# Performance work log

Hardware: AMD Instinct MI355X
Metric: run time of the kernel (lower is better)

The kernel has to match this reference:

```python
import jax, jax.numpy as jnp
import numpy as np

B, T, V, H = 4, 512, 8000, 7


def setup_inputs() -> dict:
    key = jax.random.key(0)
    k1, k2, k3 = jax.random.split(key, 3)
    return {
        "input_ids": jax.random.randint(k1, (B, T), 0, V),
        "frequencies": jax.random.normal(k2, (V,), dtype=jnp.float32) * 3.0,
        "amplitudes": 1.0 + jax.random.normal(k3, (V,), dtype=jnp.float32) * 0.1,
        "decay": jnp.asarray(1.5, dtype=jnp.float32),
        "chunk_size": 16,
    }


def reference(input_ids, frequencies, amplitudes, decay, chunk_size):
    h = jnp.arange(1, H + 1, dtype=frequencies.dtype)  # (H,)
    # harmonic expansion: freqs = f*[1..H], amps = A/[1..H]^decay
    all_f = frequencies[:, None] * h                    # (V, H)
    all_A = amplitudes[:, None] / h ** decay            # (V, H)
    seq_f = frequencies[input_ids][..., None] * h       # (B, T, H)
    seq_A = amplitudes[input_ids][..., None] / h ** decay

    nc = T // chunk_size
    sfc = seq_f.reshape(B, nc, chunk_size, H).transpose(1, 0, 2, 3)  # (nc,B,c,H)
    sAc = seq_A.reshape(B, nc, chunk_size, H).transpose(1, 0, 2, 3)

    def per_chunk(args):
        sf, sA = args  # (B,c,H)
        df = sf[:, :, :, None, None] - all_f[None, None, None, :, :]   # (B,c,H,V,H)
        amp = sA[:, :, :, None, None] * all_A[None, None, None, :, :]
        return 2.0 * (amp * jnp.sinc(2.0 * df)).sum(axis=(2, 4))       # (B,c,V)

    Cc = jax.lax.map(per_chunk, (sfc, sAc))            # (nc, B, c, V)
    C = Cc.transpose(1, 0, 2, 3).reshape(B, T, V)      # (B, T, V)

    cum = jnp.cumsum(C, axis=1)
    # logits[t] uses history 0..t-1 -> shift right by one, position 0 gets zeros
    logits = jnp.concatenate([jnp.zeros_like(cum[:, :1]), cum[:, :-1]], axis=1)
    return logits
```

## Files before the change

### kernel.cpp

```cpp
#include <hip/hip_runtime.h>
#include <math.h>


typedef float v2f __attribute__((ext_vector_type(2)));
typedef float v4f __attribute__((ext_vector_type(4)));

constexpr int cB = 4, cT = 512, cV = 8000, cH = 7;
constexpr int GT = 16;
constexpr int NSEG = cT / GT;

__device__ __forceinline__ v2f pk_add(v2f a, v2f b) {
    v2f d; asm("v_pk_add_f32 %0, %1, %2" : "=v"(d) : "v"(a), "v"(b)); return d;
}
__device__ __forceinline__ v2f pk_mul(v2f a, v2f b) {
    v2f d; asm("v_pk_mul_f32 %0, %1, %2" : "=v"(d) : "v"(a), "v"(b)); return d;
}
__device__ __forceinline__ v2f pk_fma(v2f a, v2f b, v2f c) {
    v2f d; asm("v_pk_fma_f32 %0, %1, %2, %3" : "=v"(d) : "v"(a), "v"(b), "v"(c));
    return d;
}
__device__ __forceinline__ float rfl(float x) {
    return __builtin_bit_cast(float,
        __builtin_amdgcn_readfirstlane(__builtin_bit_cast(int, x)));
}

__global__ __launch_bounds__(256) void wavelm_g(
    const int* __restrict__ ids, const float* __restrict__ freq,
    const float* __restrict__ amp, const float* __restrict__ decay_p,
    float* __restrict__ out, float* __restrict__ segsum, const int segmode)
{
    const int bs  = blockIdx.y;
    const int bt0 = bs * GT;
    if ((blockIdx.x * 256 + (int)(threadIdx.x & 192u)) * 2 >= cV) return;
    const int vh  = blockIdx.x * 256 + threadIdx.x;
    const bool valid = (vh * 2 < cV);
    const int vc = valid ? vh : 0;

    const float decay = decay_p[0];
    const float q2 = __builtin_amdgcn_exp2f(-decay);
    const float q3 = __builtin_amdgcn_exp2f(-decay * 1.5849625007f);
    const float q5 = __builtin_amdgcn_exp2f(-decay * 2.3219280949f);
    const float q7 = __builtin_amdgcn_exp2f(-decay * 2.8073549221f);
    const float rp[7] = {1.f, q2, q3, q2*q2, q5, q2*q3, q7};

    const v2f fv = *(const v2f*)(freq + (size_t)vc * 2);
    const v2f Av = *(const v2f*)(amp  + (size_t)vc * 2);
    v2f nb[cH], sBw[cH], cBw[cH];
    {
        const float xrx = fv.x - rintf(fv.x);
        const float xry = fv.y - rintf(fv.y);
        const float s1x = __builtin_amdgcn_sinf(xrx);
        const float c1x = __builtin_amdgcn_cosf(xrx);
        const float s1y = __builtin_amdgcn_sinf(xry);
        const float c1y = __builtin_amdgcn_cosf(xry);
        float sx = s1x, cx = c1x, sy = s1y, cy = c1y;
#pragma unroll
        for (int k = 0; k < cH; ++k) {
            if (k) {
                const float spx = sx, cpx = cx, spy = sy, cpy = cy;
                sx = fmaf(spx, c1x,  cpx * s1x);
                cx = fmaf(cpx, c1x, -(spx * s1x));
                sy = fmaf(spy, c1y,  cpy * s1y);
                cy = fmaf(cpy, c1y, -(spy * s1y));
            }
            const float wx = Av.x * rp[k];
            const float wy = Av.y * rp[k];
            const float wsx = wx * 0.15915494309189535f;
            const float wsy = wy * 0.15915494309189535f;
            sBw[k].x = sx * wsx;  sBw[k].y = sy * wsy;
            cBw[k].x = cx * wsx;  cBw[k].y = cy * wsy;
            nb[k].x = -(fv.x * (float)(k + 1));
            nb[k].y = -(fv.y * (float)(k + 1));
        }
    }

    v2f acc;  acc.x = 0.f;  acc.y = 0.f;

    int idc = ids[bt0];
    for (int g = 0; g < GT; ++g) {
        const int idn = (g + 1 < GT) ? ids[bt0 + g + 1] : idc;

        const float fu = freq[idc];
        const float Au = amp[idc];
        const float xru = fu - rintf(fu);
        const float s1u = rfl(__builtin_amdgcn_sinf(xru));
        const float c1u = rfl(__builtin_amdgcn_cosf(xru));

        float accx = 0.f, accy = 0.f;
        float su = s1u, cu = c1u;
#pragma unroll
        for (int i = 0; i < cH; ++i) {
            if (i) { const float sp = su, cp = cu;
                     su = fmaf(sp, c1u,  cp * s1u);
                     cu = fmaf(cp, c1u, -(sp * s1u)); }
            const float au = fu * (float)(i + 1);
            v2f ai;  ai.x = au;  ai.y = au;
            v2f d[cH], p[cH];
#pragma unroll
            for (int j = 0; j < cH; ++j) d[j] = pk_add(ai, nb[j]);
            p[0] = d[0];
#pragma unroll
            for (int j = 1; j < cH; ++j) p[j] = pk_mul(p[j-1], d[j]);
            const float ptot = p[6].x * p[6].y;
            const float rt = __builtin_amdgcn_rcpf(ptot);
            v2f r;  r.x = rt * p[6].y;  r.y = rt * p[6].x;
            v2f accS = (v2f)0.f, accC = (v2f)0.f;
#pragma unroll
            for (int j = cH - 1; j >= 1; --j) {
                const v2f inv = pk_mul(r, p[j-1]);
                accS = pk_fma(cBw[j], inv, accS);
                accC = pk_fma(sBw[j], inv, accC);
                r = pk_mul(r, d[j]);
            }
            accS = pk_fma(cBw[0], r, accS);
            accC = pk_fma(sBw[0], r, accC);
            const float tx = fmaf(su, accS.x, -(cu * accC.x));
            const float ty = fmaf(su, accS.y, -(cu * accC.y));
            accx = fmaf(rp[i], tx, accx);
            accy = fmaf(rp[i], ty, accy);
        }

        if (!(fabsf(accx) < 1e30f) || !(fabsf(accy) < 1e30f)) {
            accx = 0.f;  accy = 0.f;
            float s2 = s1u, c2 = c1u;
#pragma unroll
            for (int i = 0; i < cH; ++i) {
                if (i) { const float sp = s2, cp = c2;
                         s2 = fmaf(sp, c1u,  cp * s1u);
                         c2 = fmaf(cp, c1u, -(sp * s1u)); }
                const float au = fu * (float)(i + 1);
                float ax = 0.f, ay = 0.f;
#pragma unroll
                for (int j = 0; j < cH; ++j) {
                    const float wxx = Av.x * rp[j];
                    const float wyy = Av.y * rp[j];
                    const float dx = au + nb[j].x;
                    const float dy = au + nb[j].y;
                    const float snx = fmaf(s2, cBw[j].x, -(c2 * sBw[j].x));
                    const float sny = fmaf(s2, cBw[j].y, -(c2 * sBw[j].y));
                    float qx = snx * __builtin_amdgcn_rcpf(dx);
                    float qy = sny * __builtin_amdgcn_rcpf(dy);
                    qx = (dx == 0.f) ? wxx : qx;
                    qy = (dy == 0.f) ? wyy : qy;
                    ax += qx;  ay += qy;
                }
                accx = fmaf(rp[i], ax, accx);
                accy = fmaf(rp[i], ay, accy);
            }
        }

        if (valid) {
            const float A2 = 2.f * Au;
            v2f res;  res.x = A2 * accx;  res.y = A2 * accy;
            const size_t o = (size_t)(bt0 + g) * cV + (size_t)vh * 2;
            v2f wv;  wv.x = segmode ? acc.x : res.x;
                     wv.y = segmode ? acc.y : res.y;
            *(v2f*)(out + o) = wv;
            acc = pk_add(acc, res);
        }

        idc = idn;
    }

    if (valid && segmode)
        *(v2f*)(segsum + (size_t)bs * cV + (size_t)vh * 2) = acc;
}

__global__ __launch_bounds__(256) void wavelm_addbase(
    float* __restrict__ out, const float* __restrict__ segsum)
{
    const int btq = blockIdx.y;
    const int b  = btq >> 6;
    const int t0 = (btq & 63) * 8;
    const int seg = t0 / GT;
    if (seg == 0) return;
    const int v4 = blockIdx.x * 256 + threadIdx.x;
    if (v4 >= cV / 4) return;

    const float* sp = segsum + (size_t)b * NSEG * cV + (size_t)v4 * 4;
    v4f base;  base.x = 0.f;  base.y = 0.f;  base.z = 0.f;  base.w = 0.f;
    for (int s = 0; s < seg; ++s) {
        const v4f x = *(const v4f*)(sp + (size_t)s * cV);
        base.x += x.x;  base.y += x.y;  base.z += x.z;  base.w += x.w;
    }

    float* p = out + ((size_t)b * cT + t0) * cV + (size_t)v4 * 4;
#pragma unroll
    for (int k = 0; k < 8; ++k) {
        v4f x = *(v4f*)(p + (size_t)k * cV);
        x.x += base.x;  x.y += base.y;  x.z += base.z;  x.w += base.w;
        *(v4f*)(p + (size_t)k * cV) = x;
    }
}

__global__ __launch_bounds__(256) void wavelm_scan(float* __restrict__ out)
{
    const int g = blockIdx.x * blockDim.x + threadIdx.x;
    if (g >= cB * cV) return;
    const int b = g / cV;
    const int v = g - b * cV;
    float* p = out + (size_t)b * cT * cV + v;
    float acc = 0.f;
#pragma unroll 8
    for (int t = 0; t < cT; ++t) {
        const float c = p[(size_t)t * cV];
        p[(size_t)t * cV] = acc;
        acc += c;
    }
}

extern "C" void kernel_launch(void* const* d_in, const int* in_sizes, int n_in,
                              void* d_out, int out_size, void* d_ws, size_t ws_size,
                              hipStream_t stream)
{
    const int*   ids  = (const int*)d_in[0];
    const float* freq = (const float*)d_in[1];
    const float* amp  = (const float*)d_in[2];
    const float* dec  = (const float*)d_in[3];
    float* out = (float*)d_out;
    float* segsum = (float*)d_ws;

    const size_t seg_b = (size_t)cB * NSEG * cV * sizeof(float);
    const int segmode = (seg_b <= ws_size) ? 1 : 0;

    dim3 grid((cV / 2 + 255) / 256, cB * cT / GT);
    wavelm_g<<<grid, dim3(256), 0, stream>>>(ids, freq, amp, dec,
                                             out, segsum, segmode);

    if (segmode) {
        dim3 ab((cV / 4 + 255) / 256, cB * (cT / 8));
        wavelm_addbase<<<ab, dim3(256), 0, stream>>>(out, segsum);
    } else {
        const int nchains = cB * cV;
        wavelm_scan<<<(nchains + 255) / 256, dim3(256), 0, stream>>>(out);
    }
}
```

Before: 203.4 us.

## Fuse compute and segment-base add into one cooperative persistent kernel

Merges the per-segment compute kernel and the base-add kernel into one cooperative persistent kernel. Blocks loop over tiles, then a grid-wide sync separates the compute phase from the add-base phase, which removes a second kernel launch and the gap between launches. The add-base step now walks whole 16-step segments per tile with v2f accesses instead of 8-row v4f chunks. It adds host-side occupancy and attribute queries on every call, and falls back to the two-kernel path if the cooperative launch fails.

```diff
diff --git a/kernel.cpp b/kernel.cpp
--- a/kernel.cpp
+++ b/kernel.cpp
@@ -1,13 +1,17 @@
 #include <hip/hip_runtime.h>
+#include <hip/hip_cooperative_groups.h>
 #include <math.h>
 
 
+namespace cg = cooperative_groups;
+
 typedef float v2f __attribute__((ext_vector_type(2)));
-typedef float v4f __attribute__((ext_vector_type(4)));
 
 constexpr int cB = 4, cT = 512, cV = 8000, cH = 7;
 constexpr int GT = 16;
 constexpr int NSEG = cT / GT;
+constexpr int NXB = (cV / 2 + 255) / 256;
+constexpr int NTILE = cB * NSEG * NXB;
 
 __device__ __forceinline__ v2f pk_add(v2f a, v2f b) {
     v2f d; asm("v_pk_add_f32 %0, %1, %2" : "=v"(d) : "v"(a), "v"(b)); return d;
@@ -24,24 +28,17 @@
         __builtin_amdgcn_readfirstlane(__builtin_bit_cast(int, x)));
 }
 
-__global__ __launch_bounds__(256) void wavelm_g(
-    const int* __restrict__ ids, const float* __restrict__ freq,
-    const float* __restrict__ amp, const float* __restrict__ decay_p,
+
+__device__ __forceinline__ void tile_compute(
+    const int bs, const int xb, const int* __restrict__ ids,
+    const float* __restrict__ freq, const float* __restrict__ amp,
+    const float* __restrict__ rp,
     float* __restrict__ out, float* __restrict__ segsum, const int segmode)
 {
-    const int bs  = blockIdx.y;
     const int bt0 = bs * GT;
-    if ((blockIdx.x * 256 + (int)(threadIdx.x & 192u)) * 2 >= cV) return;
-    const int vh  = blockIdx.x * 256 + threadIdx.x;
+    const int vh  = xb * 256 + (int)threadIdx.x;
     const bool valid = (vh * 2 < cV);
     const int vc = valid ? vh : 0;
-
-    const float decay = decay_p[0];
-    const float q2 = __builtin_amdgcn_exp2f(-decay);
-    const float q3 = __builtin_amdgcn_exp2f(-decay * 1.5849625007f);
-    const float q5 = __builtin_amdgcn_exp2f(-decay * 2.3219280949f);
-    const float q7 = __builtin_amdgcn_exp2f(-decay * 2.8073549221f);
-    const float rp[7] = {1.f, q2, q3, q2*q2, q5, q2*q3, q7};
 
     const v2f fv = *(const v2f*)(freq + (size_t)vc * 2);
     const v2f Av = *(const v2f*)(amp  + (size_t)vc * 2);
@@ -166,31 +163,92 @@
         *(v2f*)(segsum + (size_t)bs * cV + (size_t)vh * 2) = acc;
 }
 
+__device__ __forceinline__ void tile_addbase(
+    const int bs, const int xb,
+    float* __restrict__ out, const float* __restrict__ segsum)
+{
+    const int b   = bs >> 5;
+    const int seg = bs & (NSEG - 1);
+    const int vh  = xb * 256 + (int)threadIdx.x;
+    const bool valid = (vh * 2 < cV);
+    const int vc = valid ? vh : 0;
+
+    const v2f* ss = (const v2f*)segsum;
+    v2f base;  base.x = 0.f;  base.y = 0.f;
+    for (int s = 0; s < seg; ++s)
+        base = pk_add(base, ss[(size_t)(b * NSEG + s) * (cV / 2) + vc]);
+
+    if (valid) {
+        v2f* op = (v2f*)out;
+        const size_t o0 = (size_t)(b * cT + seg * GT) * (cV / 2) + (size_t)vh;
+#pragma unroll
+        for (int k = 0; k < GT; ++k) {
+            v2f x = op[o0 + (size_t)k * (cV / 2)];
+            op[o0 + (size_t)k * (cV / 2)] = pk_add(x, base);
+        }
+    }
+}
+
+__device__ __forceinline__ void build_rp(const float* decay_p, float* rp)
+{
+    const float decay = decay_p[0];
+    const float q2 = __builtin_amdgcn_exp2f(-decay);
+    const float q3 = __builtin_amdgcn_exp2f(-decay * 1.5849625007f);
+    const float q5 = __builtin_amdgcn_exp2f(-decay * 2.3219280949f);
+    const float q7 = __builtin_amdgcn_exp2f(-decay * 2.8073549221f);
+    rp[0] = 1.f;  rp[1] = q2;     rp[2] = q3;  rp[3] = q2 * q2;
+    rp[4] = q5;   rp[5] = q2 * q3; rp[6] = q7;
+}
+
+
+__global__ __launch_bounds__(256) void wavelm_fused(
+    const int* __restrict__ ids, const float* __restrict__ freq,
+    const float* __restrict__ amp, const float* __restrict__ decay_p,
+    float* __restrict__ out, float* __restrict__ segsum)
+{
+    float rp[cH];
+    build_rp(decay_p, rp);
+    const int nblk = gridDim.x;
+
+    for (int t = blockIdx.x; t < NTILE; t += nblk) {
+        const int bs = t >> 4;
+        const int xb = t & (NXB - 1);
+        if ((xb * 256 + (int)(threadIdx.x & 192u)) * 2 < cV)
+            tile_compute(bs, xb, ids, freq, amp, rp, out, segsum, 1);
+    }
+
+    __threadfence();
+    cg::this_grid().sync();
+
+    for (int t = blockIdx.x; t < NTILE; t += nblk) {
+        const int bs = t >> 4;
+        const int xb = t & (NXB - 1);
+        if ((bs & (NSEG - 1)) == 0) continue;
+        if ((xb * 256 + (int)(threadIdx.x & 192u)) * 2 < cV)
+            tile_addbase(bs, xb, out, segsum);
+    }
+}
+
+
+__global__ __launch_bounds__(256) void wavelm_g(
+    const int* __restrict__ ids, const float* __restrict__ freq,
+    const float* __restrict__ amp, const float* __restrict__ decay_p,
+    float* __restrict__ out, float* __restrict__ segsum, const int segmode)
+{
+    const int bs = blockIdx.y, xb = blockIdx.x;
+    if ((xb * 256 + (int)(threadIdx.x & 192u)) * 2 >= cV) return;
+    float rp[cH];
+    build_rp(decay_p, rp);
+    tile_compute(bs, xb, ids, freq, amp, rp, out, segsum, segmode);
+}
+
 __global__ __launch_bounds__(256) void wavelm_addbase(
     float* __restrict__ out, const float* __restrict__ segsum)
 {
-    const int btq = blockIdx.y;
-    const int b  = btq >> 6;
-    const int t0 = (btq & 63) * 8;
-    const int seg = t0 / GT;
-    if (seg == 0) return;
-    const int v4 = blockIdx.x * 256 + threadIdx.x;
-    if (v4 >= cV / 4) return;
-
-    const float* sp = segsum + (size_t)b * NSEG * cV + (size_t)v4 * 4;
-    v4f base;  base.x = 0.f;  base.y = 0.f;  base.z = 0.f;  base.w = 0.f;
-    for (int s = 0; s < seg; ++s) {
-        const v4f x = *(const v4f*)(sp + (size_t)s * cV);
-        base.x += x.x;  base.y += x.y;  base.z += x.z;  base.w += x.w;
-    }
-
-    float* p = out + ((size_t)b * cT + t0) * cV + (size_t)v4 * 4;
-#pragma unroll
-    for (int k = 0; k < 8; ++k) {
-        v4f x = *(v4f*)(p + (size_t)k * cV);
-        x.x += base.x;  x.y += base.y;  x.z += base.z;  x.w += base.w;
-        *(v4f*)(p + (size_t)k * cV) = x;
-    }
+    const int bs = blockIdx.y, xb = blockIdx.x;
+    if ((bs & (NSEG - 1)) == 0) return;
+    if ((xb * 256 + (int)(threadIdx.x & 192u)) * 2 >= cV) return;
+    tile_addbase(bs, xb, out, segsum);
 }
 
 __global__ __launch_bounds__(256) void wavelm_scan(float* __restrict__ out)
@@ -223,14 +281,37 @@
     const size_t seg_b = (size_t)cB * NSEG * cV * sizeof(float);
     const int segmode = (seg_b <= ws_size) ? 1 : 0;
 
-    dim3 grid((cV / 2 + 255) / 256, cB * cT / GT);
-    wavelm_g<<<grid, dim3(256), 0, stream>>>(ids, freq, amp, dec,
-                                             out, segsum, segmode);
-
     if (segmode) {
-        dim3 ab((cV / 4 + 255) / 256, cB * (cT / 8));
-        wavelm_addbase<<<ab, dim3(256), 0, stream>>>(out, segsum);
+        int dev = 0;
+        (void)hipGetDevice(&dev);
+        int coop = 0, nbcu = 0, ncu = 0;
+        (void)hipDeviceGetAttribute(&coop, hipDeviceAttributeCooperativeLaunch, dev);
+        (void)hipOccupancyMaxActiveBlocksPerMultiprocessor(&nbcu, wavelm_fused, 256, 0);
+        (void)hipDeviceGetAttribute(&ncu, hipDeviceAttributeMultiprocessorCount, dev);
+
+        bool done = false;
+        if (coop && nbcu > 0 && ncu > 0) {
+            const int cap = nbcu * ncu;
+            const int k = (NTILE + cap - 1) / cap;
+            const int nblk = (NTILE + k - 1) / k;
+            const int* a0 = ids;  const float* a1 = freq;
+            const float* a2 = amp;  const float* a3 = dec;
+            float* a4 = out;  float* a5 = segsum;
+            void* args[6] = {&a0, &a1, &a2, &a3, &a4, &a5};
+            hipError_t e = hipLaunchCooperativeKernel(
+                wavelm_fused, dim3(nblk), dim3(256), args, 0, stream);
+            done = (e == hipSuccess);
+        }
+        if (!done) {
+            dim3 grid(NXB, cB * NSEG);
+            wavelm_g<<<grid, dim3(256), 0, stream>>>(ids, freq, amp, dec,
+                                                     out, segsum, 1);
+            wavelm_addbase<<<grid, dim3(256), 0, stream>>>(out, segsum);
+        }
     } else {
+        dim3 grid(NXB, cB * NSEG);
+        wavelm_g<<<grid, dim3(256), 0, stream>>>(ids, freq, amp, dec,
+                                                 out, (float*)d_ws, 0);
         const int nchains = cB * cV;
         wavelm_scan<<<(nchains + 255) / 256, dim3(256), 0, stream>>>(out);
     }
```

Measured after the change: 320.4 us. +57.5%, slower.

## Fuse segment-base addition into main kernel via decoupled lookback flags

Applied to the files above, without the earlier changes.

Replaces the separate add-base pass with a single persistent-order kernel. Tiles are handed out by atomic ticket and publish their segment sums with release flags. Later-segment tiles spin on the earlier flags, then add the prefix base to their own outputs while those are likely still in cache. The next id's freq/amp loads are also hoisted one iteration ahead. This trades a full second read/write of the output for spin-wait synchronisation and an extra flag-clear launch.

```diff
diff --git a/kernel.cpp b/kernel.cpp
--- a/kernel.cpp
+++ b/kernel.cpp
@@ -3,11 +3,12 @@
 
 
 typedef float v2f __attribute__((ext_vector_type(2)));
-typedef float v4f __attribute__((ext_vector_type(4)));
 
 constexpr int cB = 4, cT = 512, cV = 8000, cH = 7;
 constexpr int GT = 16;
 constexpr int NSEG = cT / GT;
+constexpr int NXB = (cV / 2 + 255) / 256;
+constexpr int NTILE = NSEG * cB * NXB;
 
 __device__ __forceinline__ v2f pk_add(v2f a, v2f b) {
     v2f d; asm("v_pk_add_f32 %0, %1, %2" : "=v"(d) : "v"(a), "v"(b)); return d;
@@ -24,24 +25,26 @@
         __builtin_amdgcn_readfirstlane(__builtin_bit_cast(int, x)));
 }
 
-__global__ __launch_bounds__(256) void wavelm_g(
-    const int* __restrict__ ids, const float* __restrict__ freq,
-    const float* __restrict__ amp, const float* __restrict__ decay_p,
-    float* __restrict__ out, float* __restrict__ segsum, const int segmode)
-{
-    const int bs  = blockIdx.y;
-    const int bt0 = bs * GT;
-    if ((blockIdx.x * 256 + (int)(threadIdx.x & 192u)) * 2 >= cV) return;
-    const int vh  = blockIdx.x * 256 + threadIdx.x;
-    const bool valid = (vh * 2 < cV);
-    const int vc = valid ? vh : 0;
-
+__device__ __forceinline__ void build_rp(const float* decay_p, float* rp)
+{
     const float decay = decay_p[0];
     const float q2 = __builtin_amdgcn_exp2f(-decay);
     const float q3 = __builtin_amdgcn_exp2f(-decay * 1.5849625007f);
     const float q5 = __builtin_amdgcn_exp2f(-decay * 2.3219280949f);
     const float q7 = __builtin_amdgcn_exp2f(-decay * 2.8073549221f);
-    const float rp[7] = {1.f, q2, q3, q2*q2, q5, q2*q3, q7};
+    rp[0] = 1.f;  rp[1] = q2;      rp[2] = q3;  rp[3] = q2 * q2;
+    rp[4] = q5;   rp[5] = q2 * q3; rp[6] = q7;
+}
+
+__device__ __forceinline__ v2f tile_compute(
+    const int bs, const int xb, const int* __restrict__ ids,
+    const float* __restrict__ freq, const float* __restrict__ amp,
+    const float* __restrict__ rp, float* __restrict__ out, const int segmode)
+{
+    const int bt0 = bs * GT;
+    const int vh  = xb * 256 + (int)threadIdx.x;
+    const bool valid = (vh * 2 < cV);
+    const int vc = valid ? vh : 0;
 
     const v2f fv = *(const v2f*)(freq + (size_t)vc * 2);
     const v2f Av = *(const v2f*)(amp  + (size_t)vc * 2);
@@ -77,11 +80,12 @@
     v2f acc;  acc.x = 0.f;  acc.y = 0.f;
 
     int idc = ids[bt0];
+    float fu = freq[idc], Au = amp[idc];
     for (int g = 0; g < GT; ++g) {
         const int idn = (g + 1 < GT) ? ids[bt0 + g + 1] : idc;
-
-        const float fu = freq[idc];
-        const float Au = amp[idc];
+        const float fn = freq[idn];
+        const float An = amp[idn];
+
         const float xru = fu - rintf(fu);
         const float s1u = rfl(__builtin_amdgcn_sinf(xru));
         const float c1u = rfl(__builtin_amdgcn_cosf(xru));
@@ -159,38 +163,101 @@
             acc = pk_add(acc, res);
         }
 
-        idc = idn;
-    }
-
-    if (valid && segmode)
-        *(v2f*)(segsum + (size_t)bs * cV + (size_t)vh * 2) = acc;
-}
-
-__global__ __launch_bounds__(256) void wavelm_addbase(
-    float* __restrict__ out, const float* __restrict__ segsum)
-{
-    const int btq = blockIdx.y;
-    const int b  = btq >> 6;
-    const int t0 = (btq & 63) * 8;
-    const int seg = t0 / GT;
+        idc = idn;  fu = fn;  Au = An;
+    }
+    return acc;
+}
+
+
+__global__ __launch_bounds__(256) void wavelm_clear(int* __restrict__ flags)
+{
+    const int i = blockIdx.x * 256 + threadIdx.x;
+    if (i < NTILE + 1) flags[i] = 0;
+}
+
+
+__global__ __launch_bounds__(256) void wavelm_g2(
+    const int* __restrict__ ids, const float* __restrict__ freq,
+    const float* __restrict__ amp, const float* __restrict__ decay_p,
+    float* __restrict__ out, float* __restrict__ segsum,
+    int* __restrict__ flags)
+{
+    __shared__ int s_t;
+    if (threadIdx.x == 0)
+        s_t = __hip_atomic_fetch_add(&flags[0], 1, __ATOMIC_RELAXED,
+                                     __HIP_MEMORY_SCOPE_AGENT);
+    __syncthreads();
+    const int t   = s_t;
+    const int xb  = t & (NXB - 1);
+    const int b   = (t >> 4) & (cB - 1);
+    const int seg = t >> 6;
+    const int bs  = b * NSEG + seg;
+
+    float rp[cH];
+    build_rp(decay_p, rp);
+
+    const int vh  = xb * 256 + (int)threadIdx.x;
+    const bool valid = (vh * 2 < cV);
+
+    v2f acc;  acc.x = 0.f;  acc.y = 0.f;
+    if ((xb * 256 + (int)(threadIdx.x & 192u)) * 2 < cV)
+        acc = tile_compute(bs, xb, ids, freq, amp, rp, out, 1);
+
+    if (valid) {
+        const size_t si = (size_t)bs * cV + (size_t)vh * 2;
+        __hip_atomic_store(&segsum[si],     acc.x, __ATOMIC_RELAXED,
+                           __HIP_MEMORY_SCOPE_AGENT);
+        __hip_atomic_store(&segsum[si + 1], acc.y, __ATOMIC_RELAXED,
+                           __HIP_MEMORY_SCOPE_AGENT);
+    }
+    __threadfence();
+    __syncthreads();
+    if (threadIdx.x == 0)
+        __hip_atomic_store(&flags[1 + t], 1, __ATOMIC_RELEASE,
+                           __HIP_MEMORY_SCOPE_AGENT);
+
     if (seg == 0) return;
-    const int v4 = blockIdx.x * 256 + threadIdx.x;
-    if (v4 >= cV / 4) return;
-
-    const float* sp = segsum + (size_t)b * NSEG * cV + (size_t)v4 * 4;
-    v4f base;  base.x = 0.f;  base.y = 0.f;  base.z = 0.f;  base.w = 0.f;
+
+    if (threadIdx.x == 0) {
+        for (int s = 0; s < seg; ++s) {
+            const int pt = (s * cB + b) * NXB + xb;
+            while (__hip_atomic_load(&flags[1 + pt], __ATOMIC_ACQUIRE,
+                                     __HIP_MEMORY_SCOPE_AGENT) == 0)
+                __builtin_amdgcn_s_sleep(8);
+        }
+    }
+    __syncthreads();
+
+    if (!valid) return;
+
+    float bx = 0.f, by = 0.f;
     for (int s = 0; s < seg; ++s) {
-        const v4f x = *(const v4f*)(sp + (size_t)s * cV);
-        base.x += x.x;  base.y += x.y;  base.z += x.z;  base.w += x.w;
-    }
-
-    float* p = out + ((size_t)b * cT + t0) * cV + (size_t)v4 * 4;
-#pragma unroll
-    for (int k = 0; k < 8; ++k) {
-        v4f x = *(v4f*)(p + (size_t)k * cV);
-        x.x += base.x;  x.y += base.y;  x.z += base.z;  x.w += base.w;
-        *(v4f*)(p + (size_t)k * cV) = x;
-    }
+        const size_t si = ((size_t)(b * NSEG + s)) * cV + (size_t)vh * 2;
+        bx += __hip_atomic_load(&segsum[si],     __ATOMIC_RELAXED,
+                                __HIP_MEMORY_SCOPE_AGENT);
+        by += __hip_atomic_load(&segsum[si + 1], __ATOMIC_RELAXED,
+                                __HIP_MEMORY_SCOPE_AGENT);
+    }
+
+    const size_t o0 = (size_t)bs * GT * cV + (size_t)vh * 2;
+    for (int g = 0; g < GT; ++g) {
+        v2f x = *(v2f*)(out + o0 + (size_t)g * cV);
+        x.x += bx;  x.y += by;
+        *(v2f*)(out + o0 + (size_t)g * cV) = x;
+    }
+}
+
+
+__global__ __launch_bounds__(256) void wavelm_g(
+    const int* __restrict__ ids, const float* __restrict__ freq,
+    const float* __restrict__ amp, const float* __restrict__ decay_p,
+    float* __restrict__ out)
+{
+    const int bs = blockIdx.y, xb = blockIdx.x;
+    if ((xb * 256 + (int)(threadIdx.x & 192u)) * 2 >= cV) return;
+    float rp[cH];
+    build_rp(decay_p, rp);
+    (void)tile_compute(bs, xb, ids, freq, amp, rp, out, 0);
 }
 
 __global__ __launch_bounds__(256) void wavelm_scan(float* __restrict__ out)
@@ -218,19 +285,19 @@
     const float* amp  = (const float*)d_in[2];
     const float* dec  = (const float*)d_in[3];
     float* out = (float*)d_out;
+
     float* segsum = (float*)d_ws;
-
-    const size_t seg_b = (size_t)cB * NSEG * cV * sizeof(float);
-    const int segmode = (seg_b <= ws_size) ? 1 : 0;
-
-    dim3 grid((cV / 2 + 255) / 256, cB * cT / GT);
-    wavelm_g<<<grid, dim3(256), 0, stream>>>(ids, freq, amp, dec,
-                                             out, segsum, segmode);
-
-    if (segmode) {
-        dim3 ab((cV / 4 + 255) / 256, cB * (cT / 8));
-        wavelm_addbase<<<ab, dim3(256), 0, stream>>>(out, segsum);
+    const size_t seg_f = (size_t)cB * NSEG * cV;
+    int* flags = (int*)(segsum + seg_f);
+    const size_t need = seg_f * sizeof(float) + (NTILE + 1) * sizeof(int);
+
+    if (need <= ws_size) {
+        wavelm_clear<<<(NTILE + 256) / 256, dim3(256), 0, stream>>>(flags);
+        wavelm_g2<<<dim3(NTILE), dim3(256), 0, stream>>>(
+            ids, freq, amp, dec, out, segsum, flags);
     } else {
+        dim3 grid(NXB, cB * NSEG);
+        wavelm_g<<<grid, dim3(256), 0, stream>>>(ids, freq, amp, dec, out);
         const int nchains = cB * cV;
         wavelm_scan<<<(nchains + 255) / 256, dim3(256), 0, stream>>>(out);
     }
```

After: 640.3 us. +214.7%, slower.
